# Optimization experiments

Hardware: AMD Instinct MI355X
Metric: run time of the kernel (lower is better)

Reference implementation:

```python
import jax, jax.numpy as jnp
import numpy as np

EMB_DIM = 512
NUM_HEADS = 8
HEAD_DIM = EMB_DIM // NUM_HEADS
BATCH = 2
SEQ = 4096


def setup_inputs() -> dict:
    key = jax.random.key(0)
    ks = jax.random.split(key, 11)
    s = 1.0 / np.sqrt(EMB_DIM)
    inp = {
        "emb": jax.random.normal(ks[0], (BATCH, SEQ, EMB_DIM), jnp.float32),
        "wq": jax.random.uniform(ks[1], (EMB_DIM, EMB_DIM), jnp.float32, -s, s),
        "bq": jax.random.uniform(ks[2], (EMB_DIM,), jnp.float32, -s, s),
        "wk": jax.random.uniform(ks[3], (EMB_DIM, EMB_DIM), jnp.float32, -s, s),
        "bk": jax.random.uniform(ks[4], (EMB_DIM,), jnp.float32, -s, s),
        "wv": jax.random.uniform(ks[5], (EMB_DIM, EMB_DIM), jnp.float32, -s, s),
        "bv": jax.random.uniform(ks[6], (EMB_DIM,), jnp.float32, -s, s),
        "wo": jax.random.uniform(ks[7], (EMB_DIM, EMB_DIM), jnp.float32, -s, s),
        "bo": jax.random.uniform(ks[8], (EMB_DIM,), jnp.float32, -s, s),
        "ln_g": jnp.ones((EMB_DIM,), jnp.float32),
        "ln_b": jnp.zeros((EMB_DIM,), jnp.float32),
    }
    return inp


def _attn(emb, wq, bq, wk, bk, wv, bv, wo, bo, ln_g, ln_b):
    B, S, E = emb.shape
    H, D = NUM_HEADS, HEAD_DIM
    # projections; torch Linear: x @ W.T + b, here w stored as [E, E] acting as W.T already
    q = (emb @ wq + bq).reshape(B, S, H, D).transpose(0, 2, 1, 3)  # [B,H,S,D]
    k = (emb @ wk + bk).reshape(B, S, H, D).transpose(0, 2, 1, 3)
    v = (emb @ wv + bv).reshape(B, S, H, D).transpose(0, 2, 1, 3)
    scores = jnp.einsum("bhqd,bhkd->bhqk", q, k) / np.sqrt(D)
    # additive causal mask, exactly as in the source: upper triangle gets -1e9
    causal = jnp.triu(jnp.ones((S, S), scores.dtype), k=1) * (-1e9)
    scores = scores + causal
    probs = jax.nn.softmax(scores, axis=-1)
    attn = jnp.einsum("bhqk,bhkd->bhqd", probs, v)  # [B,H,S,D]
    attn = attn.transpose(0, 2, 1, 3).reshape(B, S, E)
    out = attn @ wo + bo
    # residual + LayerNorm (eps=1e-5, torch default)
    x = out + emb
    mu = jnp.mean(x, axis=-1, keepdims=True)
    var = jnp.mean((x - mu) ** 2, axis=-1, keepdims=True)
    return (x - mu) * jax.lax.rsqrt(var + 1e-5) * ln_g + ln_b


def reference(emb, wq, bq, wk, bk, wv, bv, wo, bo, ln_g, ln_b):
    return _attn(emb, wq, bq, wk, bk, wv, bv, wo, bo, ln_g, ln_b)
```

## Files before the change

kernel.cpp:

```cpp
#include <hip/hip_runtime.h>

#define E 512
#define Hh 8
#define Dd 64
#define Ss 4096
#define Bb 2

typedef _Float16 f16;
typedef __attribute__((ext_vector_type(4))) _Float16 f16x4;
typedef __attribute__((ext_vector_type(8))) _Float16 f16x8;
typedef __attribute__((ext_vector_type(4))) float f32x4;

__global__ __launch_bounds__(256) void cvt_emb_kernel(const float* __restrict__ in,
                                                      f16* __restrict__ out) {
    int i = (blockIdx.x * 256 + threadIdx.x) * 8;
    float4 a = *(const float4*)(in + i);
    float4 b = *(const float4*)(in + i + 4);
    f16x8 o;
    o[0] = (f16)a.x; o[1] = (f16)a.y; o[2] = (f16)a.z; o[3] = (f16)a.w;
    o[4] = (f16)b.x; o[5] = (f16)b.y; o[6] = (f16)b.z; o[7] = (f16)b.w;
    *(f16x8*)(out + i) = o;
}

__global__ __launch_bounds__(64) void cvt_w_kernel(const float* __restrict__ wq,
                                                   const float* __restrict__ wk,
                                                   const float* __restrict__ wv,
                                                   const float* __restrict__ wo,
                                                   f16* __restrict__ wtqkv,
                                                   f16* __restrict__ wto) {
    int n = blockIdx.x;
    int t = threadIdx.x;
    const float* src;
    f16* dst;
    int col = n & 511;
    if (n < 1536) {
        int which = n >> 9;
        src = (which == 0) ? wq : (which == 1) ? wk : wv;
        dst = wtqkv + (size_t)n * E;
    } else {
        src = wo;
        dst = wto + (size_t)(n - 1536) * E;
    }
    int k0 = t * 8;
    f16x8 o;
#pragma unroll
    for (int j = 0; j < 8; ++j) o[j] = (f16)src[(size_t)(k0 + j) * E + col];
    *(f16x8*)(dst + k0) = o;
}

#define LDP 40

__global__ __launch_bounds__(256) void gemm_qkv_kernel(
    const f16* __restrict__ A, const f16* __restrict__ Wt,
    const float* __restrict__ bq, const float* __restrict__ bk,
    const float* __restrict__ bv,
    f16* __restrict__ Qb, f16* __restrict__ Kb, f16* __restrict__ Vt) {
    __shared__ f16 As[128 * LDP];
    __shared__ f16 Bs[128 * LDP];
    int tid = threadIdx.x;
    int m0 = blockIdx.x * 128, n0 = blockIdx.y * 128;
    int w = tid >> 6, lane = tid & 63;
    int wr = w >> 1, wc = w & 1;
    int lgrp = lane >> 4, l16 = lane & 15;
    f32x4 acc[4][4];
#pragma unroll
    for (int i = 0; i < 4; ++i)
#pragma unroll
        for (int j = 0; j < 4; ++j) acc[i][j] = (f32x4){0.f, 0.f, 0.f, 0.f};

    for (int kt = 0; kt < 16; ++kt) {
        int k0 = kt * 32;
        {
            int c = tid, row = c >> 2, seg = c & 3;
            *(f16x8*)&As[row * LDP + seg * 8] = *(const f16x8*)&A[(size_t)(m0 + row) * E + k0 + seg * 8];
            *(f16x8*)&Bs[row * LDP + seg * 8] = *(const f16x8*)&Wt[(size_t)(n0 + row) * E + k0 + seg * 8];
            c = tid + 256; row = c >> 2; seg = c & 3;
            *(f16x8*)&As[row * LDP + seg * 8] = *(const f16x8*)&A[(size_t)(m0 + row) * E + k0 + seg * 8];
            *(f16x8*)&Bs[row * LDP + seg * 8] = *(const f16x8*)&Wt[(size_t)(n0 + row) * E + k0 + seg * 8];
        }
        __syncthreads();
        f16x8 af[4], bfr[4];
#pragma unroll
        for (int mi = 0; mi < 4; ++mi)
            af[mi] = *(const f16x8*)&As[(wr * 64 + mi * 16 + l16) * LDP + lgrp * 8];
#pragma unroll
        for (int ni = 0; ni < 4; ++ni)
            bfr[ni] = *(const f16x8*)&Bs[(wc * 64 + ni * 16 + l16) * LDP + lgrp * 8];
#pragma unroll
        for (int mi = 0; mi < 4; ++mi)
#pragma unroll
            for (int ni = 0; ni < 4; ++ni)
                acc[mi][ni] = __builtin_amdgcn_mfma_f32_16x16x32_f16(af[mi], bfr[ni], acc[mi][ni], 0, 0, 0);
        __syncthreads();
    }
#pragma unroll
    for (int mi = 0; mi < 4; ++mi) {
#pragma unroll
        for (int ni = 0; ni < 4; ++ni) {
#pragma unroll
            for (int r = 0; r < 4; ++r) {
                int gm = m0 + wr * 64 + mi * 16 + lgrp * 4 + r;
                int gn = n0 + wc * 64 + ni * 16 + l16;
                int which = gn >> 9, e = gn & 511;
                int h = e >> 6, d = e & 63;
                int b = gm >> 12, s = gm & 4095;
                float v = acc[mi][ni][r];
                if (which == 0) {
                    v = (v + bq[e]) * 0.180336880111f;
                    Qb[(size_t)((b * Hh + h) * Ss + s) * Dd + d] = (f16)v;
                } else if (which == 1) {
                    v += bk[e];
                    Kb[(size_t)((b * Hh + h) * Ss + s) * Dd + d] = (f16)v;
                } else {
                    v += bv[e];
                    Vt[(size_t)((b * Hh + h) * Dd + d) * Ss + s] = (f16)v;
                }
            }
        }
    }
}

__global__ __launch_bounds__(64) void attn_kernel(const f16* __restrict__ Qb,
                                                  const f16* __restrict__ Kb,
                                                  const f16* __restrict__ Vt,
                                                  f16* __restrict__ attn) {
    __shared__ __align__(16) f16 Pw[32 * 64];
    __shared__ __align__(16) float sclw[32];
    int lane = threadIdx.x;
    int g = lane >> 4, l16 = lane & 15;
    int idx = blockIdx.x;
    int bh = idx & 15;
    int tile = 127 - (idx >> 4);
    int q0 = tile * 32;
    const f16* Qp = Qb + (size_t)bh * Ss * Dd;
    const f16* Kp = Kb + (size_t)bh * Ss * Dd;
    const f16* Vp = Vt + (size_t)bh * Dd * Ss;

    f16x8 qf[2][2];
#pragma unroll
    for (int nf = 0; nf < 2; ++nf)
#pragma unroll
        for (int kc = 0; kc < 2; ++kc)
            qf[nf][kc] = *(const f16x8*)&Qp[(size_t)(q0 + nf * 16 + l16) * Dd + kc * 32 + g * 8];

    f32x4 o[2][4];
#pragma unroll
    for (int mq = 0; mq < 2; ++mq)
#pragma unroll
        for (int nd = 0; nd < 4; ++nd) o[mq][nd] = (f32x4){0.f, 0.f, 0.f, 0.f};
    float m_run[2] = {-INFINITY, -INFINITY}, l_run[2] = {0.f, 0.f};

    const int count = (tile >> 1) + 1;
    for (int t = 0; t < count; ++t) {
        int n0 = t << 6;
        bool last = (t == count - 1);

        f16x8 kf[4][2];
#pragma unroll
        for (int mf = 0; mf < 4; ++mf)
#pragma unroll
            for (int kc = 0; kc < 2; ++kc)
                kf[mf][kc] = *(const f16x8*)&Kp[(size_t)(n0 + mf * 16 + l16) * Dd + kc * 32 + g * 8];

        f32x4 s_[4][2];
#pragma unroll
        for (int mf = 0; mf < 4; ++mf)
#pragma unroll
            for (int nf = 0; nf < 2; ++nf) s_[mf][nf] = (f32x4){0.f, 0.f, 0.f, 0.f};
        __builtin_amdgcn_s_setprio(1);
#pragma unroll
        for (int kc = 0; kc < 2; ++kc)
#pragma unroll
            for (int mf = 0; mf < 4; ++mf)
#pragma unroll
                for (int nf = 0; nf < 2; ++nf)
                    s_[mf][nf] = __builtin_amdgcn_mfma_f32_16x16x32_f16(kf[mf][kc], qf[nf][kc], s_[mf][nf], 0, 0, 0);
        __builtin_amdgcn_s_setprio(0);

        f16x8 vf[4][2];
#pragma unroll
        for (int nd = 0; nd < 4; ++nd)
#pragma unroll
            for (int kc = 0; kc < 2; ++kc)
                vf[nd][kc] = *(const f16x8*)&Vp[(size_t)(nd * 16 + l16) * Ss + n0 + kc * 32 + g * 8];

        if (last) {
#pragma unroll
            for (int mf = 0; mf < 4; ++mf)
#pragma unroll
                for (int nf = 0; nf < 2; ++nf)
#pragma unroll
                    for (int r = 0; r < 4; ++r) {
                        int kv = n0 + mf * 16 + 4 * g + r;
                        int qq = q0 + nf * 16 + l16;
                        if (kv > qq) s_[mf][nf][r] = -INFINITY;
                    }
        }

        float scl2[2];
#pragma unroll
        for (int nf = 0; nf < 2; ++nf) {
            float a0 = fmaxf(fmaxf(s_[0][nf][0], s_[0][nf][1]), fmaxf(s_[0][nf][2], s_[0][nf][3]));
            float a1 = fmaxf(fmaxf(s_[1][nf][0], s_[1][nf][1]), fmaxf(s_[1][nf][2], s_[1][nf][3]));
            float a2 = fmaxf(fmaxf(s_[2][nf][0], s_[2][nf][1]), fmaxf(s_[2][nf][2], s_[2][nf][3]));
            float a3 = fmaxf(fmaxf(s_[3][nf][0], s_[3][nf][1]), fmaxf(s_[3][nf][2], s_[3][nf][3]));
            float mx = fmaxf(fmaxf(a0, a1), fmaxf(a2, a3));
            mx = fmaxf(mx, __shfl_xor(mx, 16));
            mx = fmaxf(mx, __shfl_xor(mx, 32));
            float mn = fmaxf(m_run[nf], mx);
            float sc = exp2f(m_run[nf] - mn);
            float ps[4];
#pragma unroll
            for (int mf = 0; mf < 4; ++mf) {
                float p0 = exp2f(s_[mf][nf][0] - mn);
                float p1 = exp2f(s_[mf][nf][1] - mn);
                float p2 = exp2f(s_[mf][nf][2] - mn);
                float p3 = exp2f(s_[mf][nf][3] - mn);
                s_[mf][nf][0] = p0; s_[mf][nf][1] = p1;
                s_[mf][nf][2] = p2; s_[mf][nf][3] = p3;
                ps[mf] = (p0 + p1) + (p2 + p3);
            }
            float ss = (ps[0] + ps[1]) + (ps[2] + ps[3]);
            ss += __shfl_xor(ss, 16);
            ss += __shfl_xor(ss, 32);
            l_run[nf] = l_run[nf] * sc + ss;
            m_run[nf] = mn;
            scl2[nf] = sc;
        }

#pragma unroll
        for (int nf = 0; nf < 2; ++nf) {
            int row = nf * 16 + l16;
            char* base = (char*)Pw + row * 128;
            int swz = (row & 7) << 4;
#pragma unroll
            for (int mf = 0; mf < 4; ++mf) {
                f16x4 ph;
#pragma unroll
                for (int r = 0; r < 4; ++r) ph[r] = (f16)s_[mf][nf][r];
                *(f16x4*)(base + ((mf * 32 + g * 8) ^ swz)) = ph;
            }
        }
        if (lane < 16) { sclw[l16] = scl2[0]; sclw[16 + l16] = scl2[1]; }
        asm volatile("s_waitcnt lgkmcnt(0)" ::: "memory");
        __builtin_amdgcn_sched_barrier(0);

        f32x4 sr[2];
#pragma unroll
        for (int mq = 0; mq < 2; ++mq) sr[mq] = *(const f32x4*)&sclw[mq * 16 + 4 * g];
#pragma unroll
        for (int mq = 0; mq < 2; ++mq)
#pragma unroll
            for (int nd = 0; nd < 4; ++nd)
#pragma unroll
                for (int r = 0; r < 4; ++r) o[mq][nd][r] *= sr[mq][r];

        f16x8 pa[2][2];
#pragma unroll
        for (int mq = 0; mq < 2; ++mq) {
            int row = mq * 16 + l16;
            const char* base = (const char*)Pw + row * 128;
            int swz = (row & 7) << 4;
#pragma unroll
            for (int kc = 0; kc < 2; ++kc)
                pa[mq][kc] = *(const f16x8*)(base + ((kc * 64 + g * 16) ^ swz));
        }
        __builtin_amdgcn_s_setprio(1);
#pragma unroll
        for (int kc = 0; kc < 2; ++kc)
#pragma unroll
            for (int mq = 0; mq < 2; ++mq)
#pragma unroll
                for (int nd = 0; nd < 4; ++nd)
                    o[mq][nd] = __builtin_amdgcn_mfma_f32_16x16x32_f16(pa[mq][kc], vf[nd][kc], o[mq][nd], 0, 0, 0);
        __builtin_amdgcn_s_setprio(0);
        asm volatile("s_waitcnt lgkmcnt(0)" ::: "memory");
        __builtin_amdgcn_sched_barrier(0);
    }

    if (lane < 16) { sclw[l16] = l_run[0]; sclw[16 + l16] = l_run[1]; }
    asm volatile("s_waitcnt lgkmcnt(0)" ::: "memory");
    __builtin_amdgcn_sched_barrier(0);
    int b = bh >> 3, h = bh & 7;
#pragma unroll
    for (int mq = 0; mq < 2; ++mq) {
        f32x4 lr = *(const f32x4*)&sclw[mq * 16 + 4 * g];
#pragma unroll
        for (int r = 0; r < 4; ++r) {
            float inv = 1.f / lr[r];
            int srow = q0 + mq * 16 + 4 * g + r;
#pragma unroll
            for (int nd = 0; nd < 4; ++nd)
                attn[(size_t)(b * Ss + srow) * E + h * 64 + nd * 16 + l16] = (f16)(o[mq][nd][r] * inv);
        }
    }
}

__global__ __launch_bounds__(256) void gemm_out_kernel(
    const f16* __restrict__ A, const f16* __restrict__ Wt,
    const float* __restrict__ bo, const float* __restrict__ emb,
    float* __restrict__ xout) {
    __shared__ f16 As[128 * LDP];
    __shared__ f16 Bs[128 * LDP];
    int tid = threadIdx.x;
    int m0 = blockIdx.x * 128, n0 = blockIdx.y * 128;
    int w = tid >> 6, lane = tid & 63;
    int wr = w >> 1, wc = w & 1;
    int lgrp = lane >> 4, l16 = lane & 15;
    f32x4 acc[4][4];
#pragma unroll
    for (int i = 0; i < 4; ++i)
#pragma unroll
        for (int j = 0; j < 4; ++j) acc[i][j] = (f32x4){0.f, 0.f, 0.f, 0.f};

    for (int kt = 0; kt < 16; ++kt) {
        int k0 = kt * 32;
        {
            int c = tid, row = c >> 2, seg = c & 3;
            *(f16x8*)&As[row * LDP + seg * 8] = *(const f16x8*)&A[(size_t)(m0 + row) * E + k0 + seg * 8];
            *(f16x8*)&Bs[row * LDP + seg * 8] = *(const f16x8*)&Wt[(size_t)(n0 + row) * E + k0 + seg * 8];
            c = tid + 256; row = c >> 2; seg = c & 3;
            *(f16x8*)&As[row * LDP + seg * 8] = *(const f16x8*)&A[(size_t)(m0 + row) * E + k0 + seg * 8];
            *(f16x8*)&Bs[row * LDP + seg * 8] = *(const f16x8*)&Wt[(size_t)(n0 + row) * E + k0 + seg * 8];
        }
        __syncthreads();
        f16x8 af[4], bfr[4];
#pragma unroll
        for (int mi = 0; mi < 4; ++mi)
            af[mi] = *(const f16x8*)&As[(wr * 64 + mi * 16 + l16) * LDP + lgrp * 8];
#pragma unroll
        for (int ni = 0; ni < 4; ++ni)
            bfr[ni] = *(const f16x8*)&Bs[(wc * 64 + ni * 16 + l16) * LDP + lgrp * 8];
#pragma unroll
        for (int mi = 0; mi < 4; ++mi)
#pragma unroll
            for (int ni = 0; ni < 4; ++ni)
                acc[mi][ni] = __builtin_amdgcn_mfma_f32_16x16x32_f16(af[mi], bfr[ni], acc[mi][ni], 0, 0, 0);
        __syncthreads();
    }
#pragma unroll
    for (int mi = 0; mi < 4; ++mi) {
#pragma unroll
        for (int ni = 0; ni < 4; ++ni) {
#pragma unroll
            for (int r = 0; r < 4; ++r) {
                int gm = m0 + wr * 64 + mi * 16 + lgrp * 4 + r;
                int gn = n0 + wc * 64 + ni * 16 + l16;
                size_t idx = (size_t)gm * E + gn;
                xout[idx] = acc[mi][ni][r] + bo[gn] + emb[idx];
            }
        }
    }
}

__global__ __launch_bounds__(256) void ln_kernel(const float* __restrict__ x,
                                                 const float* __restrict__ g,
                                                 const float* __restrict__ b,
                                                 float* __restrict__ out) {
    int w = threadIdx.x >> 6, lane = threadIdx.x & 63;
    int row = blockIdx.x * 4 + w;
    const float* xr = x + (size_t)row * E;
    int c0 = lane * 8;
    float4 a = *(const float4*)&xr[c0];
    float4 c = *(const float4*)&xr[c0 + 4];
    float s = a.x + a.y + a.z + a.w + c.x + c.y + c.z + c.w;
    float q = a.x * a.x + a.y * a.y + a.z * a.z + a.w * a.w +
              c.x * c.x + c.y * c.y + c.z * c.z + c.w * c.w;
#pragma unroll
    for (int m = 1; m <= 32; m <<= 1) {
        s += __shfl_xor(s, m);
        q += __shfl_xor(q, m);
    }
    float mean = s * (1.f / 512.f);
    float var = q * (1.f / 512.f) - mean * mean;
    float rstd = rsqrtf(var + 1e-5f);
    float4 o1, o2;
    o1.x = (a.x - mean) * rstd * g[c0 + 0] + b[c0 + 0];
    o1.y = (a.y - mean) * rstd * g[c0 + 1] + b[c0 + 1];
    o1.z = (a.z - mean) * rstd * g[c0 + 2] + b[c0 + 2];
    o1.w = (a.w - mean) * rstd * g[c0 + 3] + b[c0 + 3];
    o2.x = (c.x - mean) * rstd * g[c0 + 4] + b[c0 + 4];
    o2.y = (c.y - mean) * rstd * g[c0 + 5] + b[c0 + 5];
    o2.z = (c.z - mean) * rstd * g[c0 + 6] + b[c0 + 6];
    o2.w = (c.w - mean) * rstd * g[c0 + 7] + b[c0 + 7];
    *(float4*)&out[(size_t)row * E + c0] = o1;
    *(float4*)&out[(size_t)row * E + c0 + 4] = o2;
}

extern "C" void kernel_launch(void* const* d_in, const int* in_sizes, int n_in,
                              void* d_out, int out_size, void* d_ws, size_t ws_size,
                              hipStream_t stream) {
    const float* emb = (const float*)d_in[0];
    const float* wq = (const float*)d_in[1];
    const float* bq = (const float*)d_in[2];
    const float* wk = (const float*)d_in[3];
    const float* bk = (const float*)d_in[4];
    const float* wv = (const float*)d_in[5];
    const float* bv = (const float*)d_in[6];
    const float* wo = (const float*)d_in[7];
    const float* bo = (const float*)d_in[8];
    const float* ln_g = (const float*)d_in[9];
    const float* ln_b = (const float*)d_in[10];
    float* out = (float*)d_out;

    char* ws = (char*)d_ws;
    f16* embh  = (f16*)(ws);
    f16* wtqkv = (f16*)(ws + 8388608);
    f16* wto   = (f16*)(ws + 9961472);
    f16* Qb    = (f16*)(ws + 10485760);
    f16* Kb    = (f16*)(ws + 18874368);
    f16* Vt    = (f16*)(ws + 27262976);
    f16* attnb = (f16*)(ws + 35651584);
    float* xbuf = (float*)(ws + 10485760);

    cvt_emb_kernel<<<dim3(2048), dim3(256), 0, stream>>>(emb, embh);
    cvt_w_kernel<<<dim3(2048), dim3(64), 0, stream>>>(wq, wk, wv, wo, wtqkv, wto);
    gemm_qkv_kernel<<<dim3(64, 12), dim3(256), 0, stream>>>(embh, wtqkv, bq, bk, bv, Qb, Kb, Vt);
    attn_kernel<<<dim3(2048), dim3(64), 0, stream>>>(Qb, Kb, Vt, attnb);
    gemm_out_kernel<<<dim3(64, 4), dim3(256), 0, stream>>>(attnb, wto, bo, emb, xbuf);
    ln_kernel<<<dim3(2048), dim3(256), 0, stream>>>(xbuf, ln_g, ln_b, out);
}
```

Measured before the change: 313.6 us.

## Use lazy softmax rescaling with threshold and defer row-sum reductions

The online softmax now skips the running-max update and the output rescale unless some tile max exceeds the running max by a threshold, and the row sums are kept per lane and reduced across lanes once at the end. It also uses the raw hardware exp2 intrinsic and drops a trailing LDS wait, and it remaps the batch-head index across blocks. The aim is to remove per-iteration cross-lane shuffles, the LDS round-trip for scale factors and the accumulator multiplies. The cost is that exponentials can reach up to 2^8 before normalisation in fp16 P, and removing the trailing wait may introduce LDS hazards between iterations.

```diff
diff --git a/kernel.cpp b/kernel.cpp
--- a/kernel.cpp
+++ b/kernel.cpp
@@ -129,12 +129,13 @@
     int lane = threadIdx.x;
     int g = lane >> 4, l16 = lane & 15;
     int idx = blockIdx.x;
-    int bh = idx & 15;
+    int bh = (idx & 7) * 2 + ((idx >> 3) & 1);
     int tile = 127 - (idx >> 4);
     int q0 = tile * 32;
     const f16* Qp = Qb + (size_t)bh * Ss * Dd;
     const f16* Kp = Kb + (size_t)bh * Ss * Dd;
     const f16* Vp = Vt + (size_t)bh * Dd * Ss;
+    const float THR = 8.0f;
 
     f16x8 qf[2][2];
 #pragma unroll
@@ -148,7 +149,8 @@
     for (int mq = 0; mq < 2; ++mq)
 #pragma unroll
         for (int nd = 0; nd < 4; ++nd) o[mq][nd] = (f32x4){0.f, 0.f, 0.f, 0.f};
-    float m_run[2] = {-INFINITY, -INFINITY}, l_run[2] = {0.f, 0.f};
+    float m_run[2] = {-1e30f, -1e30f};
+    float l_part[2] = {0.f, 0.f};
 
     const int count = (tile >> 1) + 1;
     for (int t = 0; t < count; ++t) {
@@ -197,35 +199,56 @@
                     }
         }
 
-        float scl2[2];
+        float tmax[2];
 #pragma unroll
         for (int nf = 0; nf < 2; ++nf) {
             float a0 = fmaxf(fmaxf(s_[0][nf][0], s_[0][nf][1]), fmaxf(s_[0][nf][2], s_[0][nf][3]));
             float a1 = fmaxf(fmaxf(s_[1][nf][0], s_[1][nf][1]), fmaxf(s_[1][nf][2], s_[1][nf][3]));
             float a2 = fmaxf(fmaxf(s_[2][nf][0], s_[2][nf][1]), fmaxf(s_[2][nf][2], s_[2][nf][3]));
             float a3 = fmaxf(fmaxf(s_[3][nf][0], s_[3][nf][1]), fmaxf(s_[3][nf][2], s_[3][nf][3]));
-            float mx = fmaxf(fmaxf(a0, a1), fmaxf(a2, a3));
-            mx = fmaxf(mx, __shfl_xor(mx, 16));
-            mx = fmaxf(mx, __shfl_xor(mx, 32));
-            float mn = fmaxf(m_run[nf], mx);
-            float sc = exp2f(m_run[nf] - mn);
+            tmax[nf] = fmaxf(fmaxf(a0, a1), fmaxf(a2, a3));
+        }
+
+        if (__any((tmax[0] > m_run[0] + THR) || (tmax[1] > m_run[1] + THR))) {
+            float sc[2];
+#pragma unroll
+            for (int nf = 0; nf < 2; ++nf) {
+                float mx = fmaxf(tmax[nf], __shfl_xor(tmax[nf], 16));
+                mx = fmaxf(mx, __shfl_xor(mx, 32));
+                float mn = fmaxf(m_run[nf], mx);
+                sc[nf] = __builtin_amdgcn_exp2f(m_run[nf] - mn);
+                m_run[nf] = mn;
+                l_part[nf] *= sc[nf];
+            }
+            if (lane < 16) { sclw[l16] = sc[0]; sclw[16 + l16] = sc[1]; }
+            asm volatile("s_waitcnt lgkmcnt(0)" ::: "memory");
+            __builtin_amdgcn_sched_barrier(0);
+            f32x4 sr[2];
+#pragma unroll
+            for (int mq = 0; mq < 2; ++mq) sr[mq] = *(const f32x4*)&sclw[mq * 16 + 4 * g];
+#pragma unroll
+            for (int mq = 0; mq < 2; ++mq)
+#pragma unroll
+                for (int nd = 0; nd < 4; ++nd)
+#pragma unroll
+                    for (int r = 0; r < 4; ++r) o[mq][nd][r] *= sr[mq][r];
+        }
+
+#pragma unroll
+        for (int nf = 0; nf < 2; ++nf) {
+            float mrun = m_run[nf];
             float ps[4];
 #pragma unroll
             for (int mf = 0; mf < 4; ++mf) {
-                float p0 = exp2f(s_[mf][nf][0] - mn);
-                float p1 = exp2f(s_[mf][nf][1] - mn);
-                float p2 = exp2f(s_[mf][nf][2] - mn);
-                float p3 = exp2f(s_[mf][nf][3] - mn);
+                float p0 = __builtin_amdgcn_exp2f(s_[mf][nf][0] - mrun);
+                float p1 = __builtin_amdgcn_exp2f(s_[mf][nf][1] - mrun);
+                float p2 = __builtin_amdgcn_exp2f(s_[mf][nf][2] - mrun);
+                float p3 = __builtin_amdgcn_exp2f(s_[mf][nf][3] - mrun);
                 s_[mf][nf][0] = p0; s_[mf][nf][1] = p1;
                 s_[mf][nf][2] = p2; s_[mf][nf][3] = p3;
                 ps[mf] = (p0 + p1) + (p2 + p3);
             }
-            float ss = (ps[0] + ps[1]) + (ps[2] + ps[3]);
-            ss += __shfl_xor(ss, 16);
-            ss += __shfl_xor(ss, 32);
-            l_run[nf] = l_run[nf] * sc + ss;
-            m_run[nf] = mn;
-            scl2[nf] = sc;
+            l_part[nf] += (ps[0] + ps[1]) + (ps[2] + ps[3]);
         }
 
 #pragma unroll
@@ -241,19 +264,8 @@
                 *(f16x4*)(base + ((mf * 32 + g * 8) ^ swz)) = ph;
             }
         }
-        if (lane < 16) { sclw[l16] = scl2[0]; sclw[16 + l16] = scl2[1]; }
         asm volatile("s_waitcnt lgkmcnt(0)" ::: "memory");
         __builtin_amdgcn_sched_barrier(0);
-
-        f32x4 sr[2];
-#pragma unroll
-        for (int mq = 0; mq < 2; ++mq) sr[mq] = *(const f32x4*)&sclw[mq * 16 + 4 * g];
-#pragma unroll
-        for (int mq = 0; mq < 2; ++mq)
-#pragma unroll
-            for (int nd = 0; nd < 4; ++nd)
-#pragma unroll
-                for (int r = 0; r < 4; ++r) o[mq][nd][r] *= sr[mq][r];
 
         f16x8 pa[2][2];
 #pragma unroll
@@ -274,11 +286,12 @@
                 for (int nd = 0; nd < 4; ++nd)
                     o[mq][nd] = __builtin_amdgcn_mfma_f32_16x16x32_f16(pa[mq][kc], vf[nd][kc], o[mq][nd], 0, 0, 0);
         __builtin_amdgcn_s_setprio(0);
-        asm volatile("s_waitcnt lgkmcnt(0)" ::: "memory");
-        __builtin_amdgcn_sched_barrier(0);
-    }
-
-    if (lane < 16) { sclw[l16] = l_run[0]; sclw[16 + l16] = l_run[1]; }
+    }
+
+    float l0 = l_part[0], l1 = l_part[1];
+    l0 += __shfl_xor(l0, 16); l0 += __shfl_xor(l0, 32);
+    l1 += __shfl_xor(l1, 16); l1 += __shfl_xor(l1, 32);
+    if (lane < 16) { sclw[l16] = l0; sclw[16 + l16] = l1; }
     asm volatile("s_waitcnt lgkmcnt(0)" ::: "memory");
     __builtin_amdgcn_sched_barrier(0);
     int b = bh >> 3, h = bh & 7;
```

After: 302.7 us. 1.04x faster.
